# Kernel tuning notes

Hardware: AMD Instinct MI355X
Metric: run time of the kernel (lower is better)

The kernel has to match this reference:

```python
import jax, jax.numpy as jnp
import numpy as np

B, L, D_IN = 32, 200, 64
H = 64          # hidden_size
A = 36          # attention_size
NEG_SLOPE = 0.01  # torch LeakyReLU default


def setup_inputs() -> dict:
    key = jax.random.key(0)
    ks = jax.random.split(key, 7)
    s_ln = 1.0 / np.sqrt(D_IN)
    s_w1 = 1.0 / np.sqrt(3 * H)
    s_w2 = 1.0 / np.sqrt(A)
    return {
        "x": jax.random.normal(ks[0], (B, L, D_IN), dtype=jnp.float32),
        "ln_w": jax.random.uniform(ks[1], (D_IN, H), minval=-s_ln, maxval=s_ln, dtype=jnp.float32),
        "ln_b": jax.random.uniform(ks[2], (H,), minval=-s_ln, maxval=s_ln, dtype=jnp.float32),
        "w1": jax.random.uniform(ks[3], (3 * H, A), minval=-s_w1, maxval=s_w1, dtype=jnp.float32),
        "b1": jax.random.uniform(ks[4], (A,), minval=-s_w1, maxval=s_w1, dtype=jnp.float32),
        "w2": jax.random.uniform(ks[5], (A,), minval=-s_w2, maxval=s_w2, dtype=jnp.float32),
        "b2": jax.random.uniform(ks[6], (), minval=-s_w2, maxval=s_w2, dtype=jnp.float32),
    }


def reference(x, ln_w, ln_b, w1, b1, w2, b2):
    # x: [B, L, D_in] -> h: [B, L, H]
    h = jnp.einsum("bld,dh->blh", x, ln_w) + ln_b
    Ld = h.shape[1]
    Hd = h.shape[-1]
    # The torch code concatenates (x1, x2, x1*x2) where x1[b,i,j]=h[b,j],
    # x2[b,i,j]=h[b,i]. Split w1 accordingly instead of materializing the
    # [B,L,L,3H] concat tensor.
    w1a, w1b, w1c = w1[:Hd], w1[Hd:2 * Hd], w1[2 * Hd:]
    a = jnp.einsum("bjh,ha->bja", h, w1a)          # x1 contribution (depends on j)
    c = jnp.einsum("bih,ha->bia", h, w1b)          # x2 contribution (depends on i)
    cross = jnp.einsum("bih,bjh,ha->bija", h, h, w1c)  # (x1*x2) contribution
    pre = a[:, None, :, :] + c[:, :, None, :] + cross + b1   # [B,L,L,A]
    act = jax.nn.leaky_relu(pre, negative_slope=NEG_SLOPE)
    score = jnp.einsum("bija,a->bij", act, w2) + b2          # [B,L,L]
    mask = jnp.tril(jnp.ones((Ld, Ld), dtype=score.dtype))   # causal (incl. diag)
    score = score * mask
    return jnp.einsum("bij,bjh->bih", score, h)               # [B,L,H]
```

## Files before the change

kernel.cpp:

```cpp
#include <hip/hip_runtime.h>

#define B 32
#define L 200
#define DIN 64
#define H 64
#define A 36

typedef __attribute__((ext_vector_type(8))) short short8;
typedef __attribute__((ext_vector_type(4))) float floatx4;
typedef __attribute__((ext_vector_type(8))) float floatx8;

static __device__ __forceinline__ short f2bf(float f) {
    union { float f; unsigned u; } v; v.f = f;
    unsigned r = (v.u + 0x7FFF + ((v.u >> 16) & 1)) >> 16;
    return (short)r;
}
static __device__ __forceinline__ float bf2f(short s) {
    union { unsigned u; float f; } v; v.u = ((unsigned)(unsigned short)s) << 16;
    return v.f;
}

__global__ __launch_bounds__(256) void prep_kernel(
    const float* __restrict__ x, const float* __restrict__ ln_w,
    const float* __restrict__ ln_b, const float* __restrict__ w1,
    float* __restrict__ h_out, float* __restrict__ cc_out, short* __restrict__ hb16_out,
    float* __restrict__ w1a_r, float* __restrict__ w1c_r)
{
    int wave = threadIdx.x >> 6;
    int lane = threadIdx.x & 63;
    int bl0 = __builtin_amdgcn_readfirstlane(blockIdx.x * 8 + wave * 2);
    const float* x0 = x + (size_t)bl0 * DIN;
    const float* x1 = x0 + DIN;
    float acc0 = ln_b[lane], acc1 = acc0;
    #pragma unroll
    for (int d = 0; d < DIN; ++d) {
        float w = ln_w[d * H + lane];
        acc0 = fmaf(x0[d], w, acc0);
        acc1 = fmaf(x1[d], w, acc1);
    }
    __shared__ float hrow[4][2][H];
    hrow[wave][0][lane] = acc0;
    hrow[wave][1][lane] = acc1;
    h_out[(size_t)bl0 * H + lane] = acc0;
    h_out[(size_t)(bl0 + 1) * H + lane] = acc1;
    int j0 = bl0 % L, j1 = (bl0 + 1) % L;
    hb16_out[(size_t)bl0 * H + (lane ^ ((j0 & 7) << 3))] = f2bf(acc0);
    hb16_out[(size_t)(bl0 + 1) * H + (lane ^ ((j1 & 7) << 3))] = f2bf(acc1);
    if (lane < A) {
        float s0 = 0.f, s1 = 0.f;
        #pragma unroll
        for (int hh = 0; hh < H; ++hh) {
            float w = w1[(H + hh) * A + lane];
            s0 = fmaf(hrow[wave][0][hh], w, s0);
            s1 = fmaf(hrow[wave][1][hh], w, s1);
        }
        cc_out[(size_t)bl0 * A + lane] = s0;
        cc_out[(size_t)(bl0 + 1) * A + lane] = s1;
    }
    if (blockIdx.x == 0) {
        for (int idx = threadIdx.x; idx < 2 * 3 * 64 * 8; idx += 256) {
            int e = idx & 7, ln = (idx >> 3) & 63, sn = idx >> 9;
            int s = sn / 3, n = sn - 3 * s;
            int k = s * 32 + (ln >> 4) * 8 + e;
            int c = n * 16 + (ln & 15);
            w1a_r[idx] = (c < A) ? w1[k * A + c] : 0.f;
            w1c_r[idx] = (c < A) ? w1[(2 * H + k) * A + c] : 0.f;
        }
    }
}

__global__ __launch_bounds__(256) void score_kernel(
    const float* __restrict__ h, const short* __restrict__ hb16,
    const float* __restrict__ cc, const float* __restrict__ w1a_r,
    const float* __restrict__ w1c_r, const float* __restrict__ b1,
    const float* __restrict__ w2, const float* __restrict__ b2,
    float* __restrict__ out)
{
    int blk = blockIdx.x;
    int b  = blk / 50;
    int bg = blk - b * 50;
    int wave = threadIdx.x >> 6;
    int lane = threadIdx.x & 63;
    int i = __builtin_amdgcn_readfirstlane(bg + 50 * wave);
    int l15 = lane & 15, l4 = lane >> 4;

    __shared__ __align__(16) short tile[208 * 64];
    __shared__ __align__(16) float slds[4][16];

    const short* hb16b = hb16 + (size_t)b * L * H;

    for (int c = wave; c < 26; c += 4) {
        int j = (c < 25) ? (c * 8 + (lane >> 3)) : (L - 1);
        const short* src = hb16b + (size_t)j * H + (lane & 7) * 8;
        __builtin_amdgcn_global_load_lds(
            (const __attribute__((address_space(1))) void*)src,
            (__attribute__((address_space(3))) void*)&tile[c * 512],
            16, 0, 0);
    }

    const float* hi    = h + ((size_t)b * L + i) * H;
    const float* ccrow = cc + ((size_t)b * L + i) * A;
    float b2v = b2[0];
    float w2v[3], cbv[3];
    #pragma unroll
    for (int n = 0; n < 3; ++n) {
        int c = n * 16 + l15;
        w2v[n] = (c < A) ? w2[c] : 0.f;
        cbv[n] = (c < A) ? (ccrow[c] + b1[c]) : 0.f;
    }
    short8 bfrag[2][3];
    #pragma unroll
    for (int s = 0; s < 2; ++s) {
        float hik[8];
        #pragma unroll
        for (int e = 0; e < 8; ++e) hik[e] = hi[s * 32 + l4 * 8 + e];
        #pragma unroll
        for (int n = 0; n < 3; ++n) {
            floatx8 wa = *(const floatx8*)&w1a_r[(((s * 3 + n) * 64) + lane) * 8];
            floatx8 wc = *(const floatx8*)&w1c_r[(((s * 3 + n) * 64) + lane) * 8];
            #pragma unroll
            for (int e = 0; e < 8; ++e)
                bfrag[s][n][e] = f2bf(fmaf(hik[e], wc[e], wa[e]));
        }
    }
    __syncthreads();

    float oacc[4] = {0.f, 0.f, 0.f, 0.f};
    int mmax = (i >> 4) + 1;

    for (int m = 0; m < mmax; ++m) {
        int row = m * 16 + l15;
        const short* arow = tile + row * 64;
        int sw = (row & 7) << 3;
        short8 af0 = *(const short8*)(arow + ((l4 * 8) ^ sw));
        short8 af1 = *(const short8*)(arow + ((32 + l4 * 8) ^ sw));
        floatx4 a0 = {cbv[0], cbv[0], cbv[0], cbv[0]};
        floatx4 a1 = {cbv[1], cbv[1], cbv[1], cbv[1]};
        floatx4 a2 = {cbv[2], cbv[2], cbv[2], cbv[2]};
        a0 = __builtin_amdgcn_mfma_f32_16x16x32_bf16(af0, bfrag[0][0], a0, 0, 0, 0);
        a1 = __builtin_amdgcn_mfma_f32_16x16x32_bf16(af0, bfrag[0][1], a1, 0, 0, 0);
        a2 = __builtin_amdgcn_mfma_f32_16x16x32_bf16(af0, bfrag[0][2], a2, 0, 0, 0);
        a0 = __builtin_amdgcn_mfma_f32_16x16x32_bf16(af1, bfrag[1][0], a0, 0, 0, 0);
        a1 = __builtin_amdgcn_mfma_f32_16x16x32_bf16(af1, bfrag[1][1], a1, 0, 0, 0);
        a2 = __builtin_amdgcn_mfma_f32_16x16x32_bf16(af1, bfrag[1][2], a2, 0, 0, 0);
        float sp[4];
        #pragma unroll
        for (int r = 0; r < 4; ++r) {
            float v0 = a0[r], v1 = a1[r], v2 = a2[r];
            v0 = v0 > 0.f ? v0 : 0.01f * v0;
            v1 = v1 > 0.f ? v1 : 0.01f * v1;
            v2 = v2 > 0.f ? v2 : 0.01f * v2;
            sp[r] = v0 * w2v[0] + v1 * w2v[1] + v2 * w2v[2];
        }
        #pragma unroll
        for (int d = 1; d < 16; d <<= 1) {
            #pragma unroll
            for (int r = 0; r < 4; ++r) sp[r] += __shfl_xor(sp[r], d, 64);
        }
        if (l15 == 0) {
            #pragma unroll
            for (int r = 0; r < 4; ++r) {
                int jt = m * 16 + l4 * 4 + r;
                slds[wave][l4 * 4 + r] = (jt <= i) ? sp[r] + b2v : 0.f;
            }
        }
        #pragma unroll
        for (int rb = 0; rb < 4; ++rb) {
            floatx4 sv = *(const floatx4*)&slds[wave][rb * 4];
            #pragma unroll
            for (int q = 0; q < 4; ++q) {
                int j = m * 16 + rb * 4 + q;
                short hbv = tile[j * 64 + (lane ^ ((j & 7) << 3))];
                oacc[q] = fmaf(sv[q], bf2f(hbv), oacc[q]);
            }
        }
    }

    out[((size_t)b * L + i) * H + lane] = (oacc[0] + oacc[1]) + (oacc[2] + oacc[3]);
}

extern "C" void kernel_launch(void* const* d_in, const int* in_sizes, int n_in,
                              void* d_out, int out_size, void* d_ws, size_t ws_size,
                              hipStream_t stream) {
    const float* x    = (const float*)d_in[0];
    const float* ln_w = (const float*)d_in[1];
    const float* ln_b = (const float*)d_in[2];
    const float* w1   = (const float*)d_in[3];
    const float* b1   = (const float*)d_in[4];
    const float* w2   = (const float*)d_in[5];
    const float* b2   = (const float*)d_in[6];
    float* out = (float*)d_out;

    float* h_ws   = (float*)d_ws;
    float* cc_ws  = h_ws + (size_t)B * L * H;
    short* hb16_ws = (short*)(cc_ws + (size_t)B * L * A);
    float* w1a_r  = (float*)(hb16_ws + (size_t)B * L * H);
    float* w1c_r  = w1a_r + 3072;

    prep_kernel<<<(B * L) / 8, 256, 0, stream>>>(x, ln_w, ln_b, w1, h_ws, cc_ws,
                                                 hb16_ws, w1a_r, w1c_r);
    score_kernel<<<B * 50, 256, 0, stream>>>(h_ws, hb16_ws, cc_ws, w1a_r, w1c_r,
                                             b1, w2, b2, out);
}
```

Measured before the change: 37.88 us.

## Transpose score MFMA so attention dim lies in rows, cut shuffle reduction

```diff
diff --git a/kernel.cpp b/kernel.cpp
--- a/kernel.cpp
+++ b/kernel.cpp
@@ -28,34 +28,28 @@
 {
     int wave = threadIdx.x >> 6;
     int lane = threadIdx.x & 63;
-    int bl0 = __builtin_amdgcn_readfirstlane(blockIdx.x * 8 + wave * 2);
-    const float* x0 = x + (size_t)bl0 * DIN;
-    const float* x1 = x0 + DIN;
-    float acc0 = ln_b[lane], acc1 = acc0;
+    int bl = __builtin_amdgcn_readfirstlane(blockIdx.x * 4 + wave);
+    const float* xr = x + (size_t)bl * DIN;
+    float p0 = ln_b[lane], p1 = 0.f;
     #pragma unroll
-    for (int d = 0; d < DIN; ++d) {
-        float w = ln_w[d * H + lane];
-        acc0 = fmaf(x0[d], w, acc0);
-        acc1 = fmaf(x1[d], w, acc1);
+    for (int d = 0; d < DIN; d += 2) {
+        p0 = fmaf(xr[d],     ln_w[d * H + lane],       p0);
+        p1 = fmaf(xr[d + 1], ln_w[(d + 1) * H + lane], p1);
     }
-    __shared__ float hrow[4][2][H];
-    hrow[wave][0][lane] = acc0;
-    hrow[wave][1][lane] = acc1;
-    h_out[(size_t)bl0 * H + lane] = acc0;
-    h_out[(size_t)(bl0 + 1) * H + lane] = acc1;
-    int j0 = bl0 % L, j1 = (bl0 + 1) % L;
-    hb16_out[(size_t)bl0 * H + (lane ^ ((j0 & 7) << 3))] = f2bf(acc0);
-    hb16_out[(size_t)(bl0 + 1) * H + (lane ^ ((j1 & 7) << 3))] = f2bf(acc1);
+    float acc = p0 + p1;
+    __shared__ float hrow[4][H];
+    hrow[wave][lane] = acc;
+    h_out[(size_t)bl * H + lane] = acc;
+    int j = bl % L;
+    hb16_out[(size_t)bl * H + (lane ^ ((j & 7) << 3))] = f2bf(acc);
     if (lane < A) {
         float s0 = 0.f, s1 = 0.f;
         #pragma unroll
-        for (int hh = 0; hh < H; ++hh) {
-            float w = w1[(H + hh) * A + lane];
-            s0 = fmaf(hrow[wave][0][hh], w, s0);
-            s1 = fmaf(hrow[wave][1][hh], w, s1);
+        for (int hh = 0; hh < H; hh += 2) {
+            s0 = fmaf(hrow[wave][hh],     w1[(H + hh) * A + lane],     s0);
+            s1 = fmaf(hrow[wave][hh + 1], w1[(H + hh + 1) * A + lane], s1);
         }
-        cc_out[(size_t)bl0 * A + lane] = s0;
-        cc_out[(size_t)(bl0 + 1) * A + lane] = s1;
+        cc_out[(size_t)bl * A + lane] = s0 + s1;
     }
     if (blockIdx.x == 0) {
         for (int idx = threadIdx.x; idx < 2 * 3 * 64 * 8; idx += 256) {
@@ -101,14 +95,18 @@
     const float* hi    = h + ((size_t)b * L + i) * H;
     const float* ccrow = cc + ((size_t)b * L + i) * A;
     float b2v = b2[0];
-    float w2v[3], cbv[3];
+    float w2v[3][4], cbv[3][4];
     #pragma unroll
     for (int n = 0; n < 3; ++n) {
-        int c = n * 16 + l15;
-        w2v[n] = (c < A) ? w2[c] : 0.f;
-        cbv[n] = (c < A) ? (ccrow[c] + b1[c]) : 0.f;
+        #pragma unroll
+        for (int r = 0; r < 4; ++r) {
+            int a = n * 16 + l4 * 4 + r;
+            bool av = a < A;
+            w2v[n][r] = av ? w2[a] : 0.f;
+            cbv[n][r] = av ? (ccrow[a] + b1[a]) : 0.f;
+        }
     }
-    short8 bfrag[2][3];
+    short8 afrag[2][3];
     #pragma unroll
     for (int s = 0; s < 2; ++s) {
         float hik[8];
@@ -120,7 +118,7 @@
             floatx8 wc = *(const floatx8*)&w1c_r[(((s * 3 + n) * 64) + lane) * 8];
             #pragma unroll
             for (int e = 0; e < 8; ++e)
-                bfrag[s][n][e] = f2bf(fmaf(hik[e], wc[e], wa[e]));
+                afrag[s][n][e] = f2bf(fmaf(hik[e], wc[e], wa[e]));
         }
     }
     __syncthreads();
@@ -130,40 +128,34 @@
 
     for (int m = 0; m < mmax; ++m) {
         int row = m * 16 + l15;
-        const short* arow = tile + row * 64;
-        int sw = (row & 7) << 3;
-        short8 af0 = *(const short8*)(arow + ((l4 * 8) ^ sw));
-        short8 af1 = *(const short8*)(arow + ((32 + l4 * 8) ^ sw));
-        floatx4 a0 = {cbv[0], cbv[0], cbv[0], cbv[0]};
-        floatx4 a1 = {cbv[1], cbv[1], cbv[1], cbv[1]};
-        floatx4 a2 = {cbv[2], cbv[2], cbv[2], cbv[2]};
-        a0 = __builtin_amdgcn_mfma_f32_16x16x32_bf16(af0, bfrag[0][0], a0, 0, 0, 0);
-        a1 = __builtin_amdgcn_mfma_f32_16x16x32_bf16(af0, bfrag[0][1], a1, 0, 0, 0);
-        a2 = __builtin_amdgcn_mfma_f32_16x16x32_bf16(af0, bfrag[0][2], a2, 0, 0, 0);
-        a0 = __builtin_amdgcn_mfma_f32_16x16x32_bf16(af1, bfrag[1][0], a0, 0, 0, 0);
-        a1 = __builtin_amdgcn_mfma_f32_16x16x32_bf16(af1, bfrag[1][1], a1, 0, 0, 0);
-        a2 = __builtin_amdgcn_mfma_f32_16x16x32_bf16(af1, bfrag[1][2], a2, 0, 0, 0);
-        float sp[4];
+        const short* brow = tile + row * 64;
+        int sw = (l15 & 7) << 3;
+        short8 bf0 = *(const short8*)(brow + ((l4 * 8) ^ sw));
+        short8 bf1 = *(const short8*)(brow + ((32 + l4 * 8) ^ sw));
+        floatx4 c0 = {cbv[0][0], cbv[0][1], cbv[0][2], cbv[0][3]};
+        floatx4 c1 = {cbv[1][0], cbv[1][1], cbv[1][2], cbv[1][3]};
+        floatx4 c2 = {cbv[2][0], cbv[2][1], cbv[2][2], cbv[2][3]};
+        c0 = __builtin_amdgcn_mfma_f32_16x16x32_bf16(afrag[0][0], bf0, c0, 0, 0, 0);
+        c1 = __builtin_amdgcn_mfma_f32_16x16x32_bf16(afrag[0][1], bf0, c1, 0, 0, 0);
+        c2 = __builtin_amdgcn_mfma_f32_16x16x32_bf16(afrag[0][2], bf0, c2, 0, 0, 0);
+        c0 = __builtin_amdgcn_mfma_f32_16x16x32_bf16(afrag[1][0], bf1, c0, 0, 0, 0);
+        c1 = __builtin_amdgcn_mfma_f32_16x16x32_bf16(afrag[1][1], bf1, c1, 0, 0, 0);
+        c2 = __builtin_amdgcn_mfma_f32_16x16x32_bf16(afrag[1][2], bf1, c2, 0, 0, 0);
+        float sp = 0.f;
         #pragma unroll
         for (int r = 0; r < 4; ++r) {
-            float v0 = a0[r], v1 = a1[r], v2 = a2[r];
-            v0 = v0 > 0.f ? v0 : 0.01f * v0;
-            v1 = v1 > 0.f ? v1 : 0.01f * v1;
-            v2 = v2 > 0.f ? v2 : 0.01f * v2;
-            sp[r] = v0 * w2v[0] + v1 * w2v[1] + v2 * w2v[2];
+            float v0 = c0[r], v1 = c1[r], v2 = c2[r];
+            float a0 = fmaf(0.01f, fminf(v0, 0.f), fmaxf(v0, 0.f));
+            float a1 = fmaf(0.01f, fminf(v1, 0.f), fmaxf(v1, 0.f));
+            float a2 = fmaf(0.01f, fminf(v2, 0.f), fmaxf(v2, 0.f));
+            sp = fmaf(a0, w2v[0][r], sp);
+            sp = fmaf(a1, w2v[1][r], sp);
+            sp = fmaf(a2, w2v[2][r], sp);
         }
-        #pragma unroll
-        for (int d = 1; d < 16; d <<= 1) {
-            #pragma unroll
-            for (int r = 0; r < 4; ++r) sp[r] += __shfl_xor(sp[r], d, 64);
-        }
-        if (l15 == 0) {
-            #pragma unroll
-            for (int r = 0; r < 4; ++r) {
-                int jt = m * 16 + l4 * 4 + r;
-                slds[wave][l4 * 4 + r] = (jt <= i) ? sp[r] + b2v : 0.f;
-            }
-        }
+        sp += __shfl_xor(sp, 16, 64);
+        sp += __shfl_xor(sp, 32, 64);
+        float sc = (row <= i) ? sp + b2v : 0.f;
+        if (l4 == 0) slds[wave][l15] = sc;
         #pragma unroll
         for (int rb = 0; rb < 4; ++rb) {
             floatx4 sv = *(const floatx4*)&slds[wave][rb * 4];
@@ -197,7 +189,7 @@
     float* w1a_r  = (float*)(hb16_ws + (size_t)B * L * H);
     float* w1c_r  = w1a_r + 3072;
 
-    prep_kernel<<<(B * L) / 8, 256, 0, stream>>>(x, ln_w, ln_b, w1, h_ws, cc_ws,
+    prep_kernel<<<(B * L) / 4, 256, 0, stream>>>(x, ln_w, ln_b, w1, h_ws, cc_ws,
                                                  hb16_ws, w1a_r, w1c_r);
     score_kernel<<<B * 50, 256, 0, stream>>>(h_ws, hb16_ws, cc_ws, w1a_r, w1c_r,
                                              b1, w2, b2, out);
```

New measurement: 37.76 us. About the same (-0.3%).
